# Optimization experiments

Measured on AMD Instinct MI355X. Metric: run time of the kernel, lower is better.

## Reference

```python
import jax, jax.numpy as jnp
import numpy as np

N = 100000   # nodes
E = 1600000  # edges
D = 64       # hidden_channels (heads=1, concat)
NEG_SLOPE = 0.2


def setup_inputs() -> dict:
    key = jax.random.key(0)
    ks = jax.random.split(key, 16)
    s = (1.0 / np.sqrt(D)).astype(np.float32) if hasattr(np.sqrt(D), 'astype') else 1.0 / np.sqrt(D)
    s = 1.0 / float(np.sqrt(D))
    inp = {
        "x": jax.random.normal(ks[0], (N, D), jnp.float32),
        "edge_index": jax.random.randint(ks[1], (2, E), 0, N, dtype=jnp.int32).astype(jnp.int64),
        "edge_attr": jax.random.normal(ks[2], (E, 1), jnp.float32),
        # layer 1 params (PyG GATConv, heads=1): lin, lin_edge, att_src, att_dst, att_edge, bias
        "W1":  jax.random.normal(ks[3], (D, D), jnp.float32) * s,
        "We1": jax.random.normal(ks[4], (1, D), jnp.float32) * s,
        "as1": jax.random.normal(ks[5], (D,), jnp.float32) * s,
        "ad1": jax.random.normal(ks[6], (D,), jnp.float32) * s,
        "ae1": jax.random.normal(ks[7], (D,), jnp.float32) * s,
        "b1":  jnp.zeros((D,), jnp.float32),
        # layer 2 params
        "W2":  jax.random.normal(ks[8], (D, D), jnp.float32) * s,
        "We2": jax.random.normal(ks[9], (1, D), jnp.float32) * s,
        "as2": jax.random.normal(ks[10], (D,), jnp.float32) * s,
        "ad2": jax.random.normal(ks[11], (D,), jnp.float32) * s,
        "ae2": jax.random.normal(ks[12], (D,), jnp.float32) * s,
        "b2":  jnp.zeros((D,), jnp.float32),
    }
    return inp


def _gat_layer(x, src, dst, edge_attr, W, We, a_src, a_dst, a_edge, bias):
    """PyG GATConv, heads=1, add_self_loops=False, edge_dim=1."""
    n = x.shape[0]
    h = x @ W                      # [N, D]  transformed node features
    he = edge_attr @ We            # [E, D]  transformed edge features
    # per-node attention logits, gathered per edge
    alpha = ((h * a_src).sum(-1)[src]
             + (h * a_dst).sum(-1)[dst]
             + (he * a_edge).sum(-1))               # [E]
    alpha = jax.nn.leaky_relu(alpha, NEG_SLOPE)
    # segment softmax over incoming edges of each dst node
    m = jax.ops.segment_max(alpha, dst, num_segments=n)   # [N]
    m = jnp.where(jnp.isfinite(m), m, 0.0)
    e = jnp.exp(alpha - m[dst])                            # [E]
    denom = jax.ops.segment_sum(e, dst, num_segments=n) + 1e-16
    w = e / denom[dst]                                     # [E]
    # weighted scatter-add aggregation of source features
    out = jax.ops.segment_sum(h[src] * w[:, None], dst, num_segments=n)
    return out + bias


def reference(x, edge_index, edge_attr,
              W1, We1, as1, ad1, ae1, b1,
              W2, We2, as2, ad2, ae2, b2):
    src = edge_index[0]
    dst = edge_index[1]
    h = _gat_layer(x, src, dst, edge_attr, W1, We1, as1, ad1, ae1, b1)
    h = jax.nn.relu(h)
    out = _gat_layer(h, src, dst, edge_attr, W2, We2, as2, ad2, ae2, b2)
    return out
```

## Files before the change

### kernel.cpp

```cpp
#include <hip/hip_runtime.h>
#include <hip/hip_fp16.h>
#include <stdint.h>

#define D 64
constexpr float NEG_SLOPE = 0.2f;
#define NPB_SHIFT 9
#define NPB 512
#define PCHUNK 4096

__global__ void k_ce(const float* __restrict__ We1, const float* __restrict__ ae1,
                     const float* __restrict__ We2, const float* __restrict__ ae2,
                     float* __restrict__ ce){
  int lane = threadIdx.x;
  float p1 = We1[lane] * ae1[lane];
  float p2 = We2[lane] * ae2[lane];
  #pragma unroll
  for (int off = 32; off; off >>= 1){ p1 += __shfl_xor(p1, off); p2 += __shfl_xor(p2, off); }
  if (lane == 0){ ce[0] = p1; ce[1] = p2; }
}

__global__ __launch_bounds__(256) void k_gemm_dots(
    const float* __restrict__ X, const float* __restrict__ W,
    const float* __restrict__ a_s, const float* __restrict__ a_d,
    __half* __restrict__ H, float* __restrict__ asrc, float* __restrict__ adst, int n)
{
  __shared__ float sX[4 * 512];
  int lane = threadIdx.x & 63;
  int wv   = threadIdx.x >> 6;
  float* tile = sX + wv * 512;
  int wid  = blockIdx.x * 4 + wv;
  int nw   = gridDim.x * 4;
  float Wc[64];
  #pragma unroll
  for (int k = 0; k < 64; ++k) Wc[k] = W[k * D + lane];
  float asv = a_s[lane], adv = a_d[lane];
  int ngrp = (n + 7) >> 3;
  for (int g = wid; g < ngrp; g += nw){
    int r0 = g << 3;
    if (r0 + 8 <= n){
      const float4* Xg = (const float4*)(X + (size_t)r0 * D);
      float4 t0 = Xg[lane * 2], t1 = Xg[lane * 2 + 1];
      ((float4*)tile)[lane * 2]     = t0;
      ((float4*)tile)[lane * 2 + 1] = t1;
      __builtin_amdgcn_wave_barrier();
      float acc[8];
      #pragma unroll
      for (int j = 0; j < 8; ++j) acc[j] = 0.f;
      #pragma unroll
      for (int j = 0; j < 8; ++j){
        #pragma unroll
        for (int kb = 0; kb < 16; ++kb){
          float4 xv = ((const float4*)(tile + j * 64))[kb];
          acc[j] = fmaf(xv.x, Wc[kb * 4 + 0], acc[j]);
          acc[j] = fmaf(xv.y, Wc[kb * 4 + 1], acc[j]);
          acc[j] = fmaf(xv.z, Wc[kb * 4 + 2], acc[j]);
          acc[j] = fmaf(xv.w, Wc[kb * 4 + 3], acc[j]);
        }
      }
      #pragma unroll
      for (int j = 0; j < 8; ++j) H[(size_t)(r0 + j) * D + lane] = __float2half(acc[j]);
      #pragma unroll
      for (int j = 0; j < 8; ++j){
        float ps = acc[j] * asv, pd = acc[j] * adv;
        #pragma unroll
        for (int off = 32; off; off >>= 1){ ps += __shfl_xor(ps, off); pd += __shfl_xor(pd, off); }
        if (lane == 0){ asrc[r0 + j] = ps; adst[r0 + j] = pd; }
      }
    } else {
      for (int j = 0; r0 + j < n; ++j){
        float acc = 0.f;
        #pragma unroll
        for (int kb = 0; kb < 16; ++kb){
          float4 xv = *(const float4*)(X + (size_t)(r0 + j) * D + kb * 4);
          acc = fmaf(xv.x, Wc[kb * 4 + 0], acc);
          acc = fmaf(xv.y, Wc[kb * 4 + 1], acc);
          acc = fmaf(xv.z, Wc[kb * 4 + 2], acc);
          acc = fmaf(xv.w, Wc[kb * 4 + 3], acc);
        }
        H[(size_t)(r0 + j) * D + lane] = __float2half(acc);
        float ps = acc * asv, pd = acc * adv;
        #pragma unroll
        for (int off = 32; off; off >>= 1){ ps += __shfl_xor(ps, off); pd += __shfl_xor(pd, off); }
        if (lane == 0){ asrc[r0 + j] = ps; adst[r0 + j] = pd; }
      }
    }
  }
}


__global__ __launch_bounds__(256) void k_bhist(const int* __restrict__ dst,
    int* __restrict__ C, int nchunk, int e, int nbkt){
  __shared__ int hist[256];
  int tid = threadIdx.x, c = blockIdx.x;
  if (tid < nbkt) hist[tid] = 0;
  __syncthreads();
  int c0 = c * PCHUNK;
  #pragma unroll
  for (int k = 0; k < PCHUNK / 256; ++k){
    int i = c0 + tid + (k << 8);
    if (i < e) atomicAdd(&hist[dst[i] >> NPB_SHIFT], 1);
  }
  __syncthreads();
  if (tid < nbkt) C[tid * nchunk + c] = hist[tid];
}

__global__ __launch_bounds__(512) void k_cscan(int* __restrict__ C,
    int* __restrict__ btot, int nchunk){
  __shared__ int s[512];
  int b = blockIdx.x, tid = threadIdx.x;
  int v = (tid < nchunk) ? C[b * nchunk + tid] : 0;
  s[tid] = v; __syncthreads();
  #pragma unroll
  for (int off = 1; off < 512; off <<= 1){
    int t = (tid >= off) ? s[tid - off] : 0;
    __syncthreads();
    s[tid] += t;
    __syncthreads();
  }
  if (tid < nchunk) C[b * nchunk + tid] = s[tid] - v;
  if (tid == 511) btot[b] = s[511];
}

__global__ __launch_bounds__(256) void k_bscan(const int* __restrict__ btot,
    int* __restrict__ gbase, int nbkt){
  __shared__ int s[256];
  int tid = threadIdx.x;
  int v = (tid < nbkt) ? btot[tid] : 0;
  s[tid] = v; __syncthreads();
  #pragma unroll
  for (int off = 1; off < 256; off <<= 1){
    int t = (tid >= off) ? s[tid - off] : 0;
    __syncthreads();
    s[tid] += t;
    __syncthreads();
  }
  if (tid < nbkt) gbase[tid] = s[tid] - v;
  if (tid == 255) gbase[nbkt] = s[255];
}

__global__ __launch_bounds__(256) void k_part(const int* __restrict__ src,
    const int* __restrict__ dst, const float* __restrict__ ea,
    const int* __restrict__ gbase, const int* __restrict__ C, int nchunk,
    int2* __restrict__ staging, int e, int nbkt){
  __shared__ int base[256], cnt[256];
  int tid = threadIdx.x, c = blockIdx.x;
  if (tid < nbkt){ base[tid] = gbase[tid] + C[tid * nchunk + c]; cnt[tid] = 0; }
  __syncthreads();
  int c0 = c * PCHUNK;
  int w0[PCHUNK / 256], w1[PCHUNK / 256], bk[PCHUNK / 256];
  #pragma unroll
  for (int k = 0; k < PCHUNK / 256; ++k){
    int i = c0 + tid + (k << 8);
    bk[k] = -1;
    if (i < e){
      int d = dst[i];
      bk[k] = d >> NPB_SHIFT;
      w0[k] = src[i] | ((d & (NPB - 1)) << 17);
      w1[k] = __float_as_int(ea[i]);
    }
  }
  #pragma unroll
  for (int k = 0; k < PCHUNK / 256; ++k){
    if (bk[k] >= 0){
      int pos = base[bk[k]] + atomicAdd(&cnt[bk[k]], 1);
      staging[pos] = make_int2(w0[k], w1[k]);
    }
  }
}

__global__ __launch_bounds__(512) void k_bucket(const int* __restrict__ gbase,
    const int2* __restrict__ staging, int2* __restrict__ edges,
    int* __restrict__ rowptr, int n, int nbkt){
  __shared__ int degL[NPB], sc[NPB];
  int b = blockIdx.x, tid = threadIdx.x;
  int node0 = b << NPB_SHIFT;
  int nn = min(NPB, n - node0);
  int base = gbase[b], endj = gbase[b + 1];
  degL[tid] = 0;
  __syncthreads();
  for (int j = base + tid; j < endj; j += NPB)
    atomicAdd(&degL[staging[j].x >> 17], 1);
  __syncthreads();
  int dv = degL[tid];
  sc[tid] = dv;
  __syncthreads();
  #pragma unroll
  for (int off = 1; off < NPB; off <<= 1){
    int t = (tid >= off) ? sc[tid - off] : 0;
    __syncthreads();
    sc[tid] += t;
    __syncthreads();
  }
  int ex = sc[tid] - dv;
  if (tid < nn) rowptr[node0 + tid] = base + ex;
  if (b == nbkt - 1 && tid == 0) rowptr[n] = base + sc[NPB - 1];
  __syncthreads();
  degL[tid] = ex;
  __syncthreads();
  for (int j = base + tid; j < endj; j += NPB){
    int2 w = staging[j];
    int dloc = w.x >> 17;
    int pos = base + atomicAdd(&degL[dloc], 1);
    edges[pos] = make_int2(w.x & 0x1FFFF, w.y);
  }
}

__global__ __launch_bounds__(256) void k_node_fused(
    const int* __restrict__ rowptr, const int2* __restrict__ edges,
    const float* __restrict__ asrc, const float* __restrict__ adst,
    const float* __restrict__ ce, int ce_idx,
    const __half* __restrict__ H, const float* __restrict__ bias,
    float* __restrict__ out, int n, int relu)
{
  int lane = threadIdx.x & 63;
  int wv   = threadIdx.x >> 6;
  int vbase = (blockIdx.x * 4 + wv) * 2;
  if (vbase >= n) return;
  int h  = lane >> 5;
  int li = lane & 31;
  int v  = vbase + h;
  bool vok = v < n;
  int start = 0, end = 0;
  if (vok){ start = rowptr[v]; end = rowptr[v + 1]; }
  int deg = end - start;
  int degmax = max(deg, __shfl_xor(deg, 32));
  float cev = ce[ce_idx];

  if (degmax <= 32){
    int my_s = 0; float my_e = 0.f;
    if (li < deg){
      int2 pr = edges[start + li];
      my_s = pr.x;
      float a = asrc[pr.x] + adst[v] + __int_as_float(pr.y) * cev;
      a = a > 0.f ? a : NEG_SLOPE * a;
      my_e = __expf(a);
    }
    int sub = li >> 4;
    int fq  = li & 15;
    const uint2* H2 = (const uint2*)H;
    int eb = h * 32 + sub;
    int sP[8]; float wP[8]; uint2 uP[8];
    #pragma unroll
    for (int p = 0; p < 8; ++p) sP[p] = __shfl(my_s, eb + 2 * p);
    #pragma unroll
    for (int p = 0; p < 8; ++p) uP[p] = H2[(size_t)sP[p] * 16 + fq];
    float ss = my_e;
    #pragma unroll
    for (int off = 16; off; off >>= 1) ss += __shfl_xor(ss, off);
    float inv = 1.f / (ss + 1e-16f);
    #pragma unroll
    for (int p = 0; p < 8; ++p) wP[p] = __shfl(my_e, eb + 2 * p);
    float a0 = 0.f, a1 = 0.f, a2 = 0.f, a3 = 0.f;
    #pragma unroll
    for (int p = 0; p < 8; ++p){
      __half2 q0 = *(const __half2*)&uP[p].x;
      __half2 q1 = *(const __half2*)&uP[p].y;
      float2 f0 = __half22float2(q0);
      float2 f1 = __half22float2(q1);
      a0 = fmaf(f0.x, wP[p], a0);
      a1 = fmaf(f0.y, wP[p], a1);
      a2 = fmaf(f1.x, wP[p], a2);
      a3 = fmaf(f1.y, wP[p], a3);
    }
    if (degmax > 16){
      #pragma unroll
      for (int p = 0; p < 8; ++p) sP[p] = __shfl(my_s, eb + 16 + 2 * p);
      #pragma unroll
      for (int p = 0; p < 8; ++p) uP[p] = H2[(size_t)sP[p] * 16 + fq];
      #pragma unroll
      for (int p = 0; p < 8; ++p) wP[p] = __shfl(my_e, eb + 16 + 2 * p);
      #pragma unroll
      for (int p = 0; p < 8; ++p){
        __half2 q0 = *(const __half2*)&uP[p].x;
        __half2 q1 = *(const __half2*)&uP[p].y;
        float2 f0 = __half22float2(q0);
        float2 f1 = __half22float2(q1);
        a0 = fmaf(f0.x, wP[p], a0);
        a1 = fmaf(f0.y, wP[p], a1);
        a2 = fmaf(f1.x, wP[p], a2);
        a3 = fmaf(f1.y, wP[p], a3);
      }
    }
    a0 += __shfl_xor(a0, 16);
    a1 += __shfl_xor(a1, 16);
    a2 += __shfl_xor(a2, 16);
    a3 += __shfl_xor(a3, 16);
    if (vok && li < 16){
      float4 bv = ((const float4*)bias)[li];
      float4 r;
      r.x = a0 * inv + bv.x;
      r.y = a1 * inv + bv.y;
      r.z = a2 * inv + bv.z;
      r.w = a3 * inv + bv.w;
      if (relu){
        r.x = fmaxf(r.x, 0.f); r.y = fmaxf(r.y, 0.f);
        r.z = fmaxf(r.z, 0.f); r.w = fmaxf(r.w, 0.f);
      }
      ((float4*)(out + (size_t)v * D))[li] = r;
    }
  } else {
    for (int t = 0; t < 2; ++t){
      int vv = vbase + t;
      if (vv >= n) break;
      int st = rowptr[vv], en = rowptr[vv + 1];
      int dg = en - st;
      if (dg == 0){
        float bv = bias[lane];
        float r = relu ? fmaxf(bv, 0.f) : bv;
        out[(size_t)vv * D + lane] = r;
        continue;
      }
      float adv = adst[vv];
      if (dg <= 64){
        int my_s = 0; float my_e = 0.f;
        if (lane < dg){
          int2 pr = edges[st + lane];
          my_s = pr.x;
          float a = asrc[pr.x] + adv + __int_as_float(pr.y) * cev;
          a = a > 0.f ? a : NEG_SLOPE * a;
          my_e = __expf(a);
        }
        int hf = lane >> 5;
        int fp = lane & 31;
        const __half2* Hp = (const __half2*)H;
        float ss = my_e;
        #pragma unroll
        for (int off = 32; off; off >>= 1) ss += __shfl_xor(ss, off);
        float inv = 1.f / (ss + 1e-16f);
        float accx = 0.f, accy = 0.f;
        for (int k = 0; k < dg; k += 16){
          #pragma unroll
          for (int p = 0; p < 8; ++p){
            int ix = k + 2 * p + hf; ix = ix > 63 ? 63 : ix;
            int s0 = __shfl(my_s, ix);
            float w0 = __shfl(my_e, ix);
            float2 hv = __half22float2(Hp[(size_t)s0 * 32 + fp]);
            accx = fmaf(hv.x, w0, accx);
            accy = fmaf(hv.y, w0, accy);
          }
        }
        accx += __shfl_xor(accx, 32);
        accy += __shfl_xor(accy, 32);
        if (lane < 32){
          float2 bv2 = ((const float2*)bias)[fp];
          float2 r;
          r.x = accx * inv + bv2.x;
          r.y = accy * inv + bv2.y;
          if (relu){ r.x = fmaxf(r.x, 0.f); r.y = fmaxf(r.y, 0.f); }
          ((float2*)(out + (size_t)vv * D))[fp] = r;
        }
      } else {
        float bv = bias[lane];
        float c0 = 0.f, c1 = 0.f, c2 = 0.f, c3 = 0.f;
        float ss = 0.f;
        for (int j0 = st; j0 < en; j0 += 64){
          int j = j0 + lane;
          int my_s = 0; float my_e = 0.f;
          if (j < en){
            int2 pr = edges[j];
            float a = asrc[pr.x] + adv + __int_as_float(pr.y) * cev;
            a = a > 0.f ? a : NEG_SLOPE * a;
            my_e = __expf(a);
            my_s = pr.x;
          }
          ss += my_e;
          int cnt = min(64, en - j0);
          int k = 0;
          for (; k + 4 <= cnt; k += 4){
            int s0 = __shfl(my_s, k+0), s1 = __shfl(my_s, k+1);
            int s2 = __shfl(my_s, k+2), s3 = __shfl(my_s, k+3);
            float w0 = __shfl(my_e, k+0), w1 = __shfl(my_e, k+1);
            float w2 = __shfl(my_e, k+2), w3 = __shfl(my_e, k+3);
            float h0 = __half2float(H[(size_t)s0 * D + lane]);
            float h1 = __half2float(H[(size_t)s1 * D + lane]);
            float h2 = __half2float(H[(size_t)s2 * D + lane]);
            float h3 = __half2float(H[(size_t)s3 * D + lane]);
            c0 = fmaf(h0, w0, c0); c1 = fmaf(h1, w1, c1);
            c2 = fmaf(h2, w2, c2); c3 = fmaf(h3, w3, c3);
          }
          for (; k < cnt; ++k){
            int s0 = __shfl(my_s, k);
            float w0 = __shfl(my_e, k);
            c0 = fmaf(__half2float(H[(size_t)s0 * D + lane]), w0, c0);
          }
        }
        #pragma unroll
        for (int off = 32; off; off >>= 1) ss += __shfl_xor(ss, off);
        float inv = 1.f / (ss + 1e-16f);
        float acc = (c0 + c1) + (c2 + c3);
        float r = acc * inv + bv;
        if (relu) r = fmaxf(r, 0.f);
        out[(size_t)vv * D + lane] = r;
      }
    }
  }
}

extern "C" void kernel_launch(void* const* d_in, const int* in_sizes, int n_in,
                              void* d_out, int out_size, void* d_ws, size_t ws_size,
                              hipStream_t stream)
{
  const float* x    = (const float*)d_in[0];
  const int*   ei   = (const int*)d_in[1];
  const float* ea   = (const float*)d_in[2];
  const float* W1   = (const float*)d_in[3];
  const float* We1  = (const float*)d_in[4];
  const float* as1  = (const float*)d_in[5];
  const float* ad1  = (const float*)d_in[6];
  const float* ae1  = (const float*)d_in[7];
  const float* b1   = (const float*)d_in[8];
  const float* W2   = (const float*)d_in[9];
  const float* We2  = (const float*)d_in[10];
  const float* as2  = (const float*)d_in[11];
  const float* ad2  = (const float*)d_in[12];
  const float* ae2  = (const float*)d_in[13];
  const float* b2   = (const float*)d_in[14];
  float* out = (float*)d_out;

  int n = in_sizes[0] / D;
  int e = in_sizes[1] / 2;
  const int* srcp = ei;
  const int* dstp = ei + e;

  int nbkt   = (n + NPB - 1) / NPB;
  int nchunk = (e + PCHUNK - 1) / PCHUNK;

  char* p = (char*)d_ws;
  __half* buf_h  = (__half*)p; p += (size_t)n * D * 2;
  float* buf_x2  = (float*)p;  p += (size_t)n * D * 4;
  float* asrc    = (float*)p;  p += (size_t)n * 4;
  float* adst    = (float*)p;  p += (size_t)n * 4;
  int*   rowptr  = (int*)p;    p += (size_t)(n + 16) * 4;
  int*   gbase   = (int*)p;    p += (size_t)(nbkt + 4) * 4;
  int*   btot    = (int*)p;    p += (size_t)(nbkt + 4) * 4;
  int*   C       = (int*)p;    p += (size_t)nbkt * nchunk * 4;
  float* ce      = (float*)p;  p += 64;
  int2*  edges   = (int2*)p;   p += (size_t)e * 8;
  int2*  staging = (int2*)buf_x2;

  int pairs = (n + 1) / 2;
  int gR = (pairs + 3) / 4;
  int gG = ((n + 7) / 8 + 3) / 4;

  k_ce<<<1, 64, 0, stream>>>(We1, ae1, We2, ae2, ce);
  k_bhist<<<nchunk, 256, 0, stream>>>(dstp, C, nchunk, e, nbkt);
  k_cscan<<<nbkt, 512, 0, stream>>>(C, btot, nchunk);
  k_bscan<<<1, 256, 0, stream>>>(btot, gbase, nbkt);
  k_part<<<nchunk, 256, 0, stream>>>(srcp, dstp, ea, gbase, C, nchunk, staging, e, nbkt);
  k_bucket<<<nbkt, NPB, 0, stream>>>(gbase, staging, edges, rowptr, n, nbkt);

  k_gemm_dots<<<gG, 256, 0, stream>>>(x, W1, as1, ad1, buf_h, asrc, adst, n);
  k_node_fused<<<gR, 256, 0, stream>>>(rowptr, edges, asrc, adst, ce, 0, buf_h, b1, buf_x2, n, 1);

  k_gemm_dots<<<gG, 256, 0, stream>>>(buf_x2, W2, as2, ad2, buf_h, asrc, adst, n);
  k_node_fused<<<gR, 256, 0, stream>>>(rowptr, edges, asrc, adst, ce, 1, buf_h, b2, out, n, 0);
}
```

Measured before the change: 281.5 us.

## Fuse layer-2 projection into aggregation epilogue and merge front preprocessing kernels

The first-layer aggregation kernel now keeps each node's output row in shared memory and immediately multiplies it by W2. It writes the half-precision H2 and the layer-2 attention dots directly, which drops the fp32 intermediate buffer and the second GEMM kernel. The layer-1 GEMM, the destination histogram and the edge-constant computation are merged into one launch split by block ranges. The bucket-total scan folds into the chunk-scan kernel through a last-block-done atomic counter. This cuts kernel launches and global traffic, at the cost of per-wave W2 reads from global memory inside the aggregation kernel and a larger grid-wide atomic handoff.

After: 352.0 us. 25.1% more time.

```diff
diff --git a/kernel.cpp b/kernel.cpp
--- a/kernel.cpp
+++ b/kernel.cpp
@@ -8,105 +8,111 @@
 #define NPB 512
 #define PCHUNK 4096
 
-__global__ void k_ce(const float* __restrict__ We1, const float* __restrict__ ae1,
-                     const float* __restrict__ We2, const float* __restrict__ ae2,
-                     float* __restrict__ ce){
-  int lane = threadIdx.x;
-  float p1 = We1[lane] * ae1[lane];
-  float p2 = We2[lane] * ae2[lane];
-  #pragma unroll
-  for (int off = 32; off; off >>= 1){ p1 += __shfl_xor(p1, off); p2 += __shfl_xor(p2, off); }
-  if (lane == 0){ ce[0] = p1; ce[1] = p2; }
-}
-
-__global__ __launch_bounds__(256) void k_gemm_dots(
+__global__ __launch_bounds__(256) void k_front(
     const float* __restrict__ X, const float* __restrict__ W,
     const float* __restrict__ a_s, const float* __restrict__ a_d,
-    __half* __restrict__ H, float* __restrict__ asrc, float* __restrict__ adst, int n)
+    __half* __restrict__ H, float* __restrict__ asrc, float* __restrict__ adst,
+    int n, int gemmBlocks,
+    const int* __restrict__ dst, int* __restrict__ C, int nchunk, int e, int nbkt,
+    const float* __restrict__ We1, const float* __restrict__ ae1,
+    const float* __restrict__ We2, const float* __restrict__ ae2,
+    float* __restrict__ ce, int* __restrict__ done)
 {
   __shared__ float sX[4 * 512];
-  int lane = threadIdx.x & 63;
-  int wv   = threadIdx.x >> 6;
-  float* tile = sX + wv * 512;
-  int wid  = blockIdx.x * 4 + wv;
-  int nw   = gridDim.x * 4;
-  float Wc[64];
-  #pragma unroll
-  for (int k = 0; k < 64; ++k) Wc[k] = W[k * D + lane];
-  float asv = a_s[lane], adv = a_d[lane];
-  int ngrp = (n + 7) >> 3;
-  for (int g = wid; g < ngrp; g += nw){
-    int r0 = g << 3;
-    if (r0 + 8 <= n){
-      const float4* Xg = (const float4*)(X + (size_t)r0 * D);
-      float4 t0 = Xg[lane * 2], t1 = Xg[lane * 2 + 1];
-      ((float4*)tile)[lane * 2]     = t0;
-      ((float4*)tile)[lane * 2 + 1] = t1;
-      __builtin_amdgcn_wave_barrier();
-      float acc[8];
+  int b = blockIdx.x;
+  if (b < gemmBlocks){
+    int lane = threadIdx.x & 63;
+    int wv   = threadIdx.x >> 6;
+    float* tile = sX + wv * 512;
+    int wid  = b * 4 + wv;
+    int nw   = gemmBlocks * 4;
+    float Wc[64];
+    #pragma unroll
+    for (int k = 0; k < 64; ++k) Wc[k] = W[k * D + lane];
+    float asv = a_s[lane], adv = a_d[lane];
+    int ngrp = (n + 7) >> 3;
+    for (int g = wid; g < ngrp; g += nw){
+      int r0 = g << 3;
+      if (r0 + 8 <= n){
+        const float4* Xg = (const float4*)(X + (size_t)r0 * D);
+        float4 t0 = Xg[lane * 2], t1 = Xg[lane * 2 + 1];
+        ((float4*)tile)[lane * 2]     = t0;
+        ((float4*)tile)[lane * 2 + 1] = t1;
+        __builtin_amdgcn_wave_barrier();
+        float acc[8];
+        #pragma unroll
+        for (int j = 0; j < 8; ++j) acc[j] = 0.f;
+        #pragma unroll
+        for (int j = 0; j < 8; ++j){
+          #pragma unroll
+          for (int kb = 0; kb < 16; ++kb){
+            float4 xv = ((const float4*)(tile + j * 64))[kb];
+            acc[j] = fmaf(xv.x, Wc[kb * 4 + 0], acc[j]);
+            acc[j] = fmaf(xv.y, Wc[kb * 4 + 1], acc[j]);
+            acc[j] = fmaf(xv.z, Wc[kb * 4 + 2], acc[j]);
+            acc[j] = fmaf(xv.w, Wc[kb * 4 + 3], acc[j]);
+          }
+        }
+        #pragma unroll
+        for (int j = 0; j < 8; ++j) H[(size_t)(r0 + j) * D + lane] = __float2half(acc[j]);
+        #pragma unroll
+        for (int j = 0; j < 8; ++j){
+          float ps = acc[j] * asv, pd = acc[j] * adv;
+          #pragma unroll
+          for (int off = 32; off; off >>= 1){ ps += __shfl_xor(ps, off); pd += __shfl_xor(pd, off); }
+          if (lane == 0){ asrc[r0 + j] = ps; adst[r0 + j] = pd; }
+        }
+      } else {
+        for (int j = 0; r0 + j < n; ++j){
+          float acc = 0.f;
+          #pragma unroll
+          for (int kb = 0; kb < 16; ++kb){
+            float4 xv = *(const float4*)(X + (size_t)(r0 + j) * D + kb * 4);
+            acc = fmaf(xv.x, Wc[kb * 4 + 0], acc);
+            acc = fmaf(xv.y, Wc[kb * 4 + 1], acc);
+            acc = fmaf(xv.z, Wc[kb * 4 + 2], acc);
+            acc = fmaf(xv.w, Wc[kb * 4 + 3], acc);
+          }
+          H[(size_t)(r0 + j) * D + lane] = __float2half(acc);
+          float ps = acc * asv, pd = acc * adv;
+          #pragma unroll
+          for (int off = 32; off; off >>= 1){ ps += __shfl_xor(ps, off); pd += __shfl_xor(pd, off); }
+          if (lane == 0){ asrc[r0 + j] = ps; adst[r0 + j] = pd; }
+        }
+      }
+    }
+  } else if (b < gemmBlocks + nchunk){
+    int* hist = (int*)sX;
+    int tid = threadIdx.x, c = b - gemmBlocks;
+    if (tid < nbkt) hist[tid] = 0;
+    __syncthreads();
+    int c0 = c * PCHUNK;
+    #pragma unroll
+    for (int k = 0; k < PCHUNK / 256; ++k){
+      int i = c0 + tid + (k << 8);
+      if (i < e) atomicAdd(&hist[dst[i] >> NPB_SHIFT], 1);
+    }
+    __syncthreads();
+    if (tid < nbkt) C[tid * nchunk + c] = hist[tid];
+  } else {
+    int tid = threadIdx.x;
+    if (tid < 64){
+      float p1 = We1[tid] * ae1[tid];
+      float p2 = We2[tid] * ae2[tid];
       #pragma unroll
-      for (int j = 0; j < 8; ++j) acc[j] = 0.f;
-      #pragma unroll
-      for (int j = 0; j < 8; ++j){
-        #pragma unroll
-        for (int kb = 0; kb < 16; ++kb){
-          float4 xv = ((const float4*)(tile + j * 64))[kb];
-          acc[j] = fmaf(xv.x, Wc[kb * 4 + 0], acc[j]);
-          acc[j] = fmaf(xv.y, Wc[kb * 4 + 1], acc[j]);
-          acc[j] = fmaf(xv.z, Wc[kb * 4 + 2], acc[j]);
-          acc[j] = fmaf(xv.w, Wc[kb * 4 + 3], acc[j]);
-        }
-      }
-      #pragma unroll
-      for (int j = 0; j < 8; ++j) H[(size_t)(r0 + j) * D + lane] = __float2half(acc[j]);
-      #pragma unroll
-      for (int j = 0; j < 8; ++j){
-        float ps = acc[j] * asv, pd = acc[j] * adv;
-        #pragma unroll
-        for (int off = 32; off; off >>= 1){ ps += __shfl_xor(ps, off); pd += __shfl_xor(pd, off); }
-        if (lane == 0){ asrc[r0 + j] = ps; adst[r0 + j] = pd; }
-      }
-    } else {
-      for (int j = 0; r0 + j < n; ++j){
-        float acc = 0.f;
-        #pragma unroll
-        for (int kb = 0; kb < 16; ++kb){
-          float4 xv = *(const float4*)(X + (size_t)(r0 + j) * D + kb * 4);
-          acc = fmaf(xv.x, Wc[kb * 4 + 0], acc);
-          acc = fmaf(xv.y, Wc[kb * 4 + 1], acc);
-          acc = fmaf(xv.z, Wc[kb * 4 + 2], acc);
-          acc = fmaf(xv.w, Wc[kb * 4 + 3], acc);
-        }
-        H[(size_t)(r0 + j) * D + lane] = __float2half(acc);
-        float ps = acc * asv, pd = acc * adv;
-        #pragma unroll
-        for (int off = 32; off; off >>= 1){ ps += __shfl_xor(ps, off); pd += __shfl_xor(pd, off); }
-        if (lane == 0){ asrc[r0 + j] = ps; adst[r0 + j] = pd; }
-      }
+      for (int off = 32; off; off >>= 1){ p1 += __shfl_xor(p1, off); p2 += __shfl_xor(p2, off); }
+      if (tid == 0){ ce[0] = p1; ce[1] = p2; }
+    } else if (tid == 64){
+      *done = 0;
     }
   }
 }
 
-
-__global__ __launch_bounds__(256) void k_bhist(const int* __restrict__ dst,
-    int* __restrict__ C, int nchunk, int e, int nbkt){
-  __shared__ int hist[256];
-  int tid = threadIdx.x, c = blockIdx.x;
-  if (tid < nbkt) hist[tid] = 0;
-  __syncthreads();
-  int c0 = c * PCHUNK;
-  #pragma unroll
-  for (int k = 0; k < PCHUNK / 256; ++k){
-    int i = c0 + tid + (k << 8);
-    if (i < e) atomicAdd(&hist[dst[i] >> NPB_SHIFT], 1);
-  }
-  __syncthreads();
-  if (tid < nbkt) C[tid * nchunk + c] = hist[tid];
-}
-
 __global__ __launch_bounds__(512) void k_cscan(int* __restrict__ C,
-    int* __restrict__ btot, int nchunk){
+    int* __restrict__ btot, int* __restrict__ gbase, int* __restrict__ done,
+    int nchunk, int nbkt){
   __shared__ int s[512];
+  __shared__ int amLast;
   int b = blockIdx.x, tid = threadIdx.x;
   int v = (tid < nchunk) ? C[b * nchunk + tid] : 0;
   s[tid] = v; __syncthreads();
@@ -119,23 +125,22 @@
   }
   if (tid < nchunk) C[b * nchunk + tid] = s[tid] - v;
   if (tid == 511) btot[b] = s[511];
-}
-
-__global__ __launch_bounds__(256) void k_bscan(const int* __restrict__ btot,
-    int* __restrict__ gbase, int nbkt){
-  __shared__ int s[256];
-  int tid = threadIdx.x;
-  int v = (tid < nbkt) ? btot[tid] : 0;
-  s[tid] = v; __syncthreads();
+  __threadfence();
+  if (tid == 0) amLast = (atomicAdd(done, 1) == (int)gridDim.x - 1);
+  __syncthreads();
+  if (!amLast) return;
+  __threadfence();
+  int v2 = (tid < nbkt) ? btot[tid] : 0;
+  s[tid] = v2; __syncthreads();
   #pragma unroll
-  for (int off = 1; off < 256; off <<= 1){
+  for (int off = 1; off < 512; off <<= 1){
     int t = (tid >= off) ? s[tid - off] : 0;
     __syncthreads();
     s[tid] += t;
     __syncthreads();
   }
-  if (tid < nbkt) gbase[tid] = s[tid] - v;
-  if (tid == 255) gbase[nbkt] = s[255];
+  if (tid < nbkt) gbase[tid] = s[tid] - v2;
+  if (tid == 511) gbase[nbkt] = s[511];
 }
 
 __global__ __launch_bounds__(256) void k_part(const int* __restrict__ src,
@@ -210,8 +215,12 @@
     const float* __restrict__ asrc, const float* __restrict__ adst,
     const float* __restrict__ ce, int ce_idx,
     const __half* __restrict__ H, const float* __restrict__ bias,
-    float* __restrict__ out, int n, int relu)
+    float* __restrict__ out, int n, int relu,
+    const float* __restrict__ Wn, const float* __restrict__ a_sn,
+    const float* __restrict__ a_dn, __half* __restrict__ Hn,
+    float* __restrict__ asrcn, float* __restrict__ adstn)
 {
+  __shared__ float rowL[4][2][64];
   int lane = threadIdx.x & 63;
   int wv   = threadIdx.x >> 6;
   int vbase = (blockIdx.x * 4 + wv) * 2;
@@ -285,7 +294,7 @@
     a1 += __shfl_xor(a1, 16);
     a2 += __shfl_xor(a2, 16);
     a3 += __shfl_xor(a3, 16);
-    if (vok && li < 16){
+    if (li < 16){
       float4 bv = ((const float4*)bias)[li];
       float4 r;
       r.x = a0 * inv + bv.x;
@@ -296,7 +305,11 @@
         r.x = fmaxf(r.x, 0.f); r.y = fmaxf(r.y, 0.f);
         r.z = fmaxf(r.z, 0.f); r.w = fmaxf(r.w, 0.f);
       }
-      ((float4*)(out + (size_t)v * D))[li] = r;
+      if (Wn){
+        *(float4*)&rowL[wv][h][li * 4] = r;
+      } else if (vok){
+        ((float4*)(out + (size_t)v * D))[li] = r;
+      }
     }
   } else {
     for (int t = 0; t < 2; ++t){
@@ -307,7 +320,8 @@
       if (dg == 0){
         float bv = bias[lane];
         float r = relu ? fmaxf(bv, 0.f) : bv;
-        out[(size_t)vv * D + lane] = r;
+        if (Wn) rowL[wv][t][lane] = r;
+        else    out[(size_t)vv * D + lane] = r;
         continue;
       }
       float adv = adst[vv];
@@ -347,7 +361,11 @@
           r.x = accx * inv + bv2.x;
           r.y = accy * inv + bv2.y;
           if (relu){ r.x = fmaxf(r.x, 0.f); r.y = fmaxf(r.y, 0.f); }
-          ((float2*)(out + (size_t)vv * D))[fp] = r;
+          if (Wn){
+            *(float2*)&rowL[wv][t][fp * 2] = r;
+          } else {
+            ((float2*)(out + (size_t)vv * D))[fp] = r;
+          }
         }
       } else {
         float bv = bias[lane];
@@ -390,8 +408,38 @@
         float acc = (c0 + c1) + (c2 + c3);
         float r = acc * inv + bv;
         if (relu) r = fmaxf(r, 0.f);
-        out[(size_t)vv * D + lane] = r;
+        if (Wn) rowL[wv][t][lane] = r;
+        else    out[(size_t)vv * D + lane] = r;
       }
+    }
+  }
+
+  if (Wn){
+    __builtin_amdgcn_wave_barrier();
+    const float2* W2f2 = (const float2*)Wn;
+    const float4* rowq = (const float4*)rowL[wv][h];
+    float cx = 0.f, cy = 0.f;
+    #pragma unroll
+    for (int db = 0; db < 16; ++db){
+      float4 rq = rowq[db];
+      float2 wa = W2f2[(db * 4 + 0) * 32 + li];
+      float2 wb = W2f2[(db * 4 + 1) * 32 + li];
+      float2 wc = W2f2[(db * 4 + 2) * 32 + li];
+      float2 wd = W2f2[(db * 4 + 3) * 32 + li];
+      cx = fmaf(rq.x, wa.x, cx); cy = fmaf(rq.x, wa.y, cy);
+      cx = fmaf(rq.y, wb.x, cx); cy = fmaf(rq.y, wb.y, cy);
+      cx = fmaf(rq.z, wc.x, cx); cy = fmaf(rq.z, wc.y, cy);
+      cx = fmaf(rq.w, wd.x, cx); cy = fmaf(rq.w, wd.y, cy);
+    }
+    float2 av = ((const float2*)a_sn)[li];
+    float2 dv = ((const float2*)a_dn)[li];
+    float ps = cx * av.x + cy * av.y;
+    float pd = cx * dv.x + cy * dv.y;
+    #pragma unroll
+    for (int off = 16; off; off >>= 1){ ps += __shfl_xor(ps, off); pd += __shfl_xor(pd, off); }
+    if (vok){
+      ((__half2*)Hn)[(size_t)v * 32 + li] = __floats2half2_rn(cx, cy);
+      if (li == 0){ asrcn[v] = ps; adstn[v] = pd; }
     }
   }
 }
@@ -426,32 +474,34 @@
   int nchunk = (e + PCHUNK - 1) / PCHUNK;
 
   char* p = (char*)d_ws;
-  __half* buf_h  = (__half*)p; p += (size_t)n * D * 2;
-  float* buf_x2  = (float*)p;  p += (size_t)n * D * 4;
-  float* asrc    = (float*)p;  p += (size_t)n * 4;
-  float* adst    = (float*)p;  p += (size_t)n * 4;
+  __half* buf_h1 = (__half*)p; p += (size_t)n * D * 2;
+  __half* buf_h2 = (__half*)p; p += (size_t)n * D * 2;
+  float* asrc1   = (float*)p;  p += (size_t)n * 4;
+  float* adst1   = (float*)p;  p += (size_t)n * 4;
+  float* asrc2   = (float*)p;  p += (size_t)n * 4;
+  float* adst2   = (float*)p;  p += (size_t)n * 4;
   int*   rowptr  = (int*)p;    p += (size_t)(n + 16) * 4;
   int*   gbase   = (int*)p;    p += (size_t)(nbkt + 4) * 4;
   int*   btot    = (int*)p;    p += (size_t)(nbkt + 4) * 4;
   int*   C       = (int*)p;    p += (size_t)nbkt * nchunk * 4;
   float* ce      = (float*)p;  p += 64;
+  int*   done    = (int*)p;    p += 64;
   int2*  edges   = (int2*)p;   p += (size_t)e * 8;
-  int2*  staging = (int2*)buf_x2;
+  int2*  staging = (int2*)buf_h2;
 
   int pairs = (n + 1) / 2;
   int gR = (pairs + 3) / 4;
   int gG = ((n + 7) / 8 + 3) / 4;
 
-  k_ce<<<1, 64, 0, stream>>>(We1, ae1, We2, ae2, ce);
-  k_bhist<<<nchunk, 256, 0, stream>>>(dstp, C, nchunk, e, nbkt);
-  k_cscan<<<nbkt, 512, 0, stream>>>(C, btot, nchunk);
-  k_bscan<<<1, 256, 0, stream>>>(btot, gbase, nbkt);
+  k_front<<<gG + nchunk + 1, 256, 0, stream>>>(
+      x, W1, as1, ad1, buf_h1, asrc1, adst1, n, gG,
+      dstp, C, nchunk, e, nbkt, We1, ae1, We2, ae2, ce, done);
+  k_cscan<<<nbkt, 512, 0, stream>>>(C, btot, gbase, done, nchunk, nbkt);
   k_part<<<nchunk, 256, 0, stream>>>(srcp, dstp, ea, gbase, C, nchunk, staging, e, nbkt);
   k_bucket<<<nbkt, NPB, 0, stream>>>(gbase, staging, edges, rowptr, n, nbkt);
 
-  k_gemm_dots<<<gG, 256, 0, stream>>>(x, W1, as1, ad1, buf_h, asrc, adst, n);
-  k_node_fused<<<gR, 256, 0, stream>>>(rowptr, edges, asrc, adst, ce, 0, buf_h, b1, buf_x2, n, 1);
-
-  k_gemm_dots<<<gG, 256, 0, stream>>>(buf_x2, W2, as2, ad2, buf_h, asrc, adst, n);
-  k_node_fused<<<gR, 256, 0, stream>>>(rowptr, edges, asrc, adst, ce, 1, buf_h, b2, out, n, 0);
+  k_node_fused<<<gR, 256, 0, stream>>>(rowptr, edges, asrc1, adst1, ce, 0,
+      buf_h1, b1, nullptr, n, 1, W2, as2, ad2, buf_h2, asrc2, adst2);
+  k_node_fused<<<gR, 256, 0, stream>>>(rowptr, edges, asrc2, adst2, ce, 1,
+      buf_h2, b2, out, n, 0, nullptr, nullptr, nullptr, nullptr, nullptr, nullptr);
 }
```

## Replace two-level bucket partition CSR build with global atomic degree count and scatter

Applied to the files above, without the earlier changes.

Replaces the bucketed CSR construction (per-chunk histograms, chunk scan, partition into staging, per-bucket local sort) with a simpler pipeline. The new pipeline zeroes a degree array, counts degrees with global atomics, runs a two-pass decoupled scan whose last block finishes the block sums, and scatters edges using global atomic cursors. It is meant to cut the staging round-trip and several kernel launches. In exchange it relies on many contended global atomics with random scatter writes, and the order of edges within a row becomes nondeterministic, which can change floating-point summation order.

Result: slower. 455.4 us (+61.8%).

```diff
diff --git a/kernel.cpp b/kernel.cpp
--- a/kernel.cpp
+++ b/kernel.cpp
@@ -4,19 +4,100 @@
 
 #define D 64
 constexpr float NEG_SLOPE = 0.2f;
-#define NPB_SHIFT 9
-#define NPB 512
-#define PCHUNK 4096
-
-__global__ void k_ce(const float* __restrict__ We1, const float* __restrict__ ae1,
-                     const float* __restrict__ We2, const float* __restrict__ ae2,
-                     float* __restrict__ ce){
-  int lane = threadIdx.x;
-  float p1 = We1[lane] * ae1[lane];
-  float p2 = We2[lane] * ae2[lane];
+
+__global__ __launch_bounds__(256) void k_init(
+    int* __restrict__ deg, int n, int* __restrict__ done,
+    const float* __restrict__ We1, const float* __restrict__ ae1,
+    const float* __restrict__ We2, const float* __restrict__ ae2,
+    float* __restrict__ ce)
+{
+  int i = blockIdx.x * 256 + threadIdx.x;
+  int stride = gridDim.x * 256;
+  for (; i < n; i += stride) deg[i] = 0;
+  if (blockIdx.x == 0){
+    int tid = threadIdx.x;
+    if (tid < 64){
+      float p1 = We1[tid] * ae1[tid];
+      float p2 = We2[tid] * ae2[tid];
+      #pragma unroll
+      for (int off = 32; off; off >>= 1){ p1 += __shfl_xor(p1, off); p2 += __shfl_xor(p2, off); }
+      if (tid == 0){ ce[0] = p1; ce[1] = p2; }
+    } else if (tid == 64){
+      *done = 0;
+    }
+  }
+}
+
+__global__ __launch_bounds__(256) void k_deg(const int* __restrict__ dst,
+    int* __restrict__ deg, int e)
+{
+  int i = blockIdx.x * 256 + threadIdx.x;
+  int stride = gridDim.x * 256;
+  for (; i < e; i += stride) atomicAdd(&deg[dst[i]], 1);
+}
+
+__global__ __launch_bounds__(512) void k_scan1(const int* __restrict__ deg,
+    int* __restrict__ rowptr, int* __restrict__ bsum, int* __restrict__ done,
+    int n, int nblk)
+{
+  __shared__ int s[512];
+  __shared__ int amLast;
+  int b = blockIdx.x, tid = threadIdx.x;
+  int v = b * 512 + tid;
+  int val = (v < n) ? deg[v] : 0;
+  s[tid] = val; __syncthreads();
   #pragma unroll
-  for (int off = 32; off; off >>= 1){ p1 += __shfl_xor(p1, off); p2 += __shfl_xor(p2, off); }
-  if (lane == 0){ ce[0] = p1; ce[1] = p2; }
+  for (int off = 1; off < 512; off <<= 1){
+    int t = (tid >= off) ? s[tid - off] : 0;
+    __syncthreads();
+    s[tid] += t;
+    __syncthreads();
+  }
+  if (v < n) rowptr[v] = s[tid] - val;
+  if (tid == 511) bsum[b] = s[511];
+  __threadfence();
+  if (tid == 0) amLast = (atomicAdd(done, 1) == nblk - 1);
+  __syncthreads();
+  if (!amLast) return;
+  __threadfence();
+  int v2 = (tid < nblk) ? bsum[tid] : 0;
+  s[tid] = v2; __syncthreads();
+  #pragma unroll
+  for (int off = 1; off < 512; off <<= 1){
+    int t = (tid >= off) ? s[tid - off] : 0;
+    __syncthreads();
+    s[tid] += t;
+    __syncthreads();
+  }
+  if (tid < nblk) bsum[tid] = s[tid] - v2;
+}
+
+__global__ __launch_bounds__(512) void k_scan2(int* __restrict__ rowptr,
+    int* __restrict__ cursor, const int* __restrict__ bsum, int n, int e)
+{
+  int b = blockIdx.x, tid = threadIdx.x;
+  int v = b * 512 + tid;
+  if (v < n){
+    int r = rowptr[v] + bsum[b];
+    rowptr[v] = r;
+    cursor[v] = r;
+  }
+  if (b == 0 && tid == 0) rowptr[n] = e;
+}
+
+__global__ __launch_bounds__(256) void k_scatter(const int* __restrict__ src,
+    const int* __restrict__ dst, const float* __restrict__ ea,
+    int* __restrict__ cursor, int2* __restrict__ edges, int e)
+{
+  int i = blockIdx.x * 256 + threadIdx.x;
+  int stride = gridDim.x * 256;
+  for (; i < e; i += stride){
+    int d = dst[i];
+    int sv = src[i];
+    float av = ea[i];
+    int pos = atomicAdd(&cursor[d], 1);
+    edges[pos] = make_int2(sv, __float_as_int(av));
+  }
 }
 
 __global__ __launch_bounds__(256) void k_gemm_dots(
@@ -84,124 +165,6 @@
         if (lane == 0){ asrc[r0 + j] = ps; adst[r0 + j] = pd; }
       }
     }
-  }
-}
-
-
-__global__ __launch_bounds__(256) void k_bhist(const int* __restrict__ dst,
-    int* __restrict__ C, int nchunk, int e, int nbkt){
-  __shared__ int hist[256];
-  int tid = threadIdx.x, c = blockIdx.x;
-  if (tid < nbkt) hist[tid] = 0;
-  __syncthreads();
-  int c0 = c * PCHUNK;
-  #pragma unroll
-  for (int k = 0; k < PCHUNK / 256; ++k){
-    int i = c0 + tid + (k << 8);
-    if (i < e) atomicAdd(&hist[dst[i] >> NPB_SHIFT], 1);
-  }
-  __syncthreads();
-  if (tid < nbkt) C[tid * nchunk + c] = hist[tid];
-}
-
-__global__ __launch_bounds__(512) void k_cscan(int* __restrict__ C,
-    int* __restrict__ btot, int nchunk){
-  __shared__ int s[512];
-  int b = blockIdx.x, tid = threadIdx.x;
-  int v = (tid < nchunk) ? C[b * nchunk + tid] : 0;
-  s[tid] = v; __syncthreads();
-  #pragma unroll
-  for (int off = 1; off < 512; off <<= 1){
-    int t = (tid >= off) ? s[tid - off] : 0;
-    __syncthreads();
-    s[tid] += t;
-    __syncthreads();
-  }
-  if (tid < nchunk) C[b * nchunk + tid] = s[tid] - v;
-  if (tid == 511) btot[b] = s[511];
-}
-
-__global__ __launch_bounds__(256) void k_bscan(const int* __restrict__ btot,
-    int* __restrict__ gbase, int nbkt){
-  __shared__ int s[256];
-  int tid = threadIdx.x;
-  int v = (tid < nbkt) ? btot[tid] : 0;
-  s[tid] = v; __syncthreads();
-  #pragma unroll
-  for (int off = 1; off < 256; off <<= 1){
-    int t = (tid >= off) ? s[tid - off] : 0;
-    __syncthreads();
-    s[tid] += t;
-    __syncthreads();
-  }
-  if (tid < nbkt) gbase[tid] = s[tid] - v;
-  if (tid == 255) gbase[nbkt] = s[255];
-}
-
-__global__ __launch_bounds__(256) void k_part(const int* __restrict__ src,
-    const int* __restrict__ dst, const float* __restrict__ ea,
-    const int* __restrict__ gbase, const int* __restrict__ C, int nchunk,
-    int2* __restrict__ staging, int e, int nbkt){
-  __shared__ int base[256], cnt[256];
-  int tid = threadIdx.x, c = blockIdx.x;
-  if (tid < nbkt){ base[tid] = gbase[tid] + C[tid * nchunk + c]; cnt[tid] = 0; }
-  __syncthreads();
-  int c0 = c * PCHUNK;
-  int w0[PCHUNK / 256], w1[PCHUNK / 256], bk[PCHUNK / 256];
-  #pragma unroll
-  for (int k = 0; k < PCHUNK / 256; ++k){
-    int i = c0 + tid + (k << 8);
-    bk[k] = -1;
-    if (i < e){
-      int d = dst[i];
-      bk[k] = d >> NPB_SHIFT;
-      w0[k] = src[i] | ((d & (NPB - 1)) << 17);
-      w1[k] = __float_as_int(ea[i]);
-    }
-  }
-  #pragma unroll
-  for (int k = 0; k < PCHUNK / 256; ++k){
-    if (bk[k] >= 0){
-      int pos = base[bk[k]] + atomicAdd(&cnt[bk[k]], 1);
-      staging[pos] = make_int2(w0[k], w1[k]);
-    }
-  }
-}
-
-__global__ __launch_bounds__(512) void k_bucket(const int* __restrict__ gbase,
-    const int2* __restrict__ staging, int2* __restrict__ edges,
-    int* __restrict__ rowptr, int n, int nbkt){
-  __shared__ int degL[NPB], sc[NPB];
-  int b = blockIdx.x, tid = threadIdx.x;
-  int node0 = b << NPB_SHIFT;
-  int nn = min(NPB, n - node0);
-  int base = gbase[b], endj = gbase[b + 1];
-  degL[tid] = 0;
-  __syncthreads();
-  for (int j = base + tid; j < endj; j += NPB)
-    atomicAdd(&degL[staging[j].x >> 17], 1);
-  __syncthreads();
-  int dv = degL[tid];
-  sc[tid] = dv;
-  __syncthreads();
-  #pragma unroll
-  for (int off = 1; off < NPB; off <<= 1){
-    int t = (tid >= off) ? sc[tid - off] : 0;
-    __syncthreads();
-    sc[tid] += t;
-    __syncthreads();
-  }
-  int ex = sc[tid] - dv;
-  if (tid < nn) rowptr[node0 + tid] = base + ex;
-  if (b == nbkt - 1 && tid == 0) rowptr[n] = base + sc[NPB - 1];
-  __syncthreads();
-  degL[tid] = ex;
-  __syncthreads();
-  for (int j = base + tid; j < endj; j += NPB){
-    int2 w = staging[j];
-    int dloc = w.x >> 17;
-    int pos = base + atomicAdd(&degL[dloc], 1);
-    edges[pos] = make_int2(w.x & 0x1FFFF, w.y);
   }
 }
 
@@ -422,8 +385,7 @@
   const int* srcp = ei;
   const int* dstp = ei + e;
 
-  int nbkt   = (n + NPB - 1) / NPB;
-  int nchunk = (e + PCHUNK - 1) / PCHUNK;
+  int nblk = (n + 511) / 512;
 
   char* p = (char*)d_ws;
   __half* buf_h  = (__half*)p; p += (size_t)n * D * 2;
@@ -431,27 +393,27 @@
   float* asrc    = (float*)p;  p += (size_t)n * 4;
   float* adst    = (float*)p;  p += (size_t)n * 4;
   int*   rowptr  = (int*)p;    p += (size_t)(n + 16) * 4;
-  int*   gbase   = (int*)p;    p += (size_t)(nbkt + 4) * 4;
-  int*   btot    = (int*)p;    p += (size_t)(nbkt + 4) * 4;
-  int*   C       = (int*)p;    p += (size_t)nbkt * nchunk * 4;
+  int*   deg     = (int*)p;    p += (size_t)(n + 16) * 4;
+  int*   cursor  = (int*)p;    p += (size_t)(n + 16) * 4;
+  int*   bsum    = (int*)p;    p += 512 * 4;
   float* ce      = (float*)p;  p += 64;
+  int*   done    = (int*)p;    p += 64;
   int2*  edges   = (int2*)p;   p += (size_t)e * 8;
-  int2*  staging = (int2*)buf_x2;
 
   int pairs = (n + 1) / 2;
   int gR = (pairs + 3) / 4;
   int gG = ((n + 7) / 8 + 3) / 4;
 
-  k_ce<<<1, 64, 0, stream>>>(We1, ae1, We2, ae2, ce);
-  k_bhist<<<nchunk, 256, 0, stream>>>(dstp, C, nchunk, e, nbkt);
-  k_cscan<<<nbkt, 512, 0, stream>>>(C, btot, nchunk);
-  k_bscan<<<1, 256, 0, stream>>>(btot, gbase, nbkt);
-  k_part<<<nchunk, 256, 0, stream>>>(srcp, dstp, ea, gbase, C, nchunk, staging, e, nbkt);
-  k_bucket<<<nbkt, NPB, 0, stream>>>(gbase, staging, edges, rowptr, n, nbkt);
+  k_init<<<256, 256, 0, stream>>>(deg, n, done, We1, ae1, We2, ae2, ce);
+  k_deg<<<1024, 256, 0, stream>>>(dstp, deg, e);
+  k_scan1<<<nblk, 512, 0, stream>>>(deg, rowptr, bsum, done, n, nblk);
+  k_scan2<<<nblk, 512, 0, stream>>>(rowptr, cursor, bsum, n, e);
+  k_scatter<<<1024, 256, 0, stream>>>(srcp, dstp, ea, cursor, edges, e);
 
   k_gemm_dots<<<gG, 256, 0, stream>>>(x, W1, as1, ad1, buf_h, asrc, adst, n);
-  k_node_fused<<<gR, 256, 0, stream>>>(rowptr, edges, asrc, adst, ce, 0, buf_h, b1, buf_x2, n, 1);
-
+  k_node_fused<<<gR, 256, 0, stream>>>(rowptr, edges, asrc, adst, ce, 0,
+      buf_h, b1, buf_x2, n, 1);
   k_gemm_dots<<<gG, 256, 0, stream>>>(buf_x2, W2, as2, ad2, buf_h, asrc, adst, n);
-  k_node_fused<<<gR, 256, 0, stream>>>(rowptr, edges, asrc, adst, ce, 1, buf_h, b2, out, n, 0);
-}
+  k_node_fused<<<gR, 256, 0, stream>>>(rowptr, edges, asrc, adst, ce, 1,
+      buf_h, b2, out, n, 0);
+}
```

## Map four nodes per wavefront in aggregation and widen partition blocks to 512

Applied to the files above, without the earlier changes.

The fused GAT aggregation kernel now gives each node 16 lanes, so one wavefront handles four destination nodes instead of two. Each lane owns a fixed 4-feature slice and walks edges serially in groups of eight. This removes the cross-half reduction and halves the number of waves. In exchange, the long-tail branch for degrees above 16 or 32 fires more often, because it is now decided by the maximum degree over four nodes. Separately, the histogram and partition kernels use 512-thread blocks with fewer items per thread.

Measured after the change: 284.1 us. About the same (+0.9%).

```diff
diff --git a/kernel.cpp b/kernel.cpp
--- a/kernel.cpp
+++ b/kernel.cpp
@@ -88,7 +88,7 @@
 }
 
 
-__global__ __launch_bounds__(256) void k_bhist(const int* __restrict__ dst,
+__global__ __launch_bounds__(512) void k_bhist(const int* __restrict__ dst,
     int* __restrict__ C, int nchunk, int e, int nbkt){
   __shared__ int hist[256];
   int tid = threadIdx.x, c = blockIdx.x;
@@ -96,8 +96,8 @@
   __syncthreads();
   int c0 = c * PCHUNK;
   #pragma unroll
-  for (int k = 0; k < PCHUNK / 256; ++k){
-    int i = c0 + tid + (k << 8);
+  for (int k = 0; k < PCHUNK / 512; ++k){
+    int i = c0 + tid + (k << 9);
     if (i < e) atomicAdd(&hist[dst[i] >> NPB_SHIFT], 1);
   }
   __syncthreads();
@@ -138,7 +138,7 @@
   if (tid == 255) gbase[nbkt] = s[255];
 }
 
-__global__ __launch_bounds__(256) void k_part(const int* __restrict__ src,
+__global__ __launch_bounds__(512) void k_part(const int* __restrict__ src,
     const int* __restrict__ dst, const float* __restrict__ ea,
     const int* __restrict__ gbase, const int* __restrict__ C, int nchunk,
     int2* __restrict__ staging, int e, int nbkt){
@@ -147,10 +147,10 @@
   if (tid < nbkt){ base[tid] = gbase[tid] + C[tid * nchunk + c]; cnt[tid] = 0; }
   __syncthreads();
   int c0 = c * PCHUNK;
-  int w0[PCHUNK / 256], w1[PCHUNK / 256], bk[PCHUNK / 256];
-  #pragma unroll
-  for (int k = 0; k < PCHUNK / 256; ++k){
-    int i = c0 + tid + (k << 8);
+  int w0[PCHUNK / 512], w1[PCHUNK / 512], bk[PCHUNK / 512];
+  #pragma unroll
+  for (int k = 0; k < PCHUNK / 512; ++k){
+    int i = c0 + tid + (k << 9);
     bk[k] = -1;
     if (i < e){
       int d = dst[i];
@@ -160,7 +160,7 @@
     }
   }
   #pragma unroll
-  for (int k = 0; k < PCHUNK / 256; ++k){
+  for (int k = 0; k < PCHUNK / 512; ++k){
     if (bk[k] >= 0){
       int pos = base[bk[k]] + atomicAdd(&cnt[bk[k]], 1);
       staging[pos] = make_int2(w0[k], w1[k]);
@@ -214,78 +214,115 @@
 {
   int lane = threadIdx.x & 63;
   int wv   = threadIdx.x >> 6;
-  int vbase = (blockIdx.x * 4 + wv) * 2;
+  int vbase = (blockIdx.x * 4 + wv) * 4;
   if (vbase >= n) return;
-  int h  = lane >> 5;
-  int li = lane & 31;
-  int v  = vbase + h;
+  int q  = lane >> 4;
+  int li = lane & 15;
+  int v  = vbase + q;
   bool vok = v < n;
   int start = 0, end = 0;
   if (vok){ start = rowptr[v]; end = rowptr[v + 1]; }
   int deg = end - start;
-  int degmax = max(deg, __shfl_xor(deg, 32));
+  int dm = deg;
+  dm = max(dm, __shfl_xor(dm, 16));
+  dm = max(dm, __shfl_xor(dm, 32));
   float cev = ce[ce_idx];
 
-  if (degmax <= 32){
-    int my_s = 0; float my_e = 0.f;
+  if (dm <= 32){
+    int s0 = 0, s1 = 0; float e0 = 0.f, e1 = 0.f;
     if (li < deg){
       int2 pr = edges[start + li];
-      my_s = pr.x;
+      s0 = pr.x;
       float a = asrc[pr.x] + adst[v] + __int_as_float(pr.y) * cev;
       a = a > 0.f ? a : NEG_SLOPE * a;
-      my_e = __expf(a);
-    }
-    int sub = li >> 4;
-    int fq  = li & 15;
+      e0 = __expf(a);
+    }
+    if (li + 16 < deg){
+      int2 pr = edges[start + 16 + li];
+      s1 = pr.x;
+      float a = asrc[pr.x] + adst[v] + __int_as_float(pr.y) * cev;
+      a = a > 0.f ? a : NEG_SLOPE * a;
+      e1 = __expf(a);
+    }
     const uint2* H2 = (const uint2*)H;
-    int eb = h * 32 + sub;
-    int sP[8]; float wP[8]; uint2 uP[8];
-    #pragma unroll
-    for (int p = 0; p < 8; ++p) sP[p] = __shfl(my_s, eb + 2 * p);
-    #pragma unroll
-    for (int p = 0; p < 8; ++p) uP[p] = H2[(size_t)sP[p] * 16 + fq];
-    float ss = my_e;
-    #pragma unroll
-    for (int off = 16; off; off >>= 1) ss += __shfl_xor(ss, off);
+    int qb = q << 4;
+    int sP[8]; uint2 uP[8]; float wP[8];
+    float a0 = 0.f, a1 = 0.f, a2 = 0.f, a3 = 0.f;
+    #pragma unroll
+    for (int p = 0; p < 8; ++p) sP[p] = __shfl(s0, qb + p);
+    #pragma unroll
+    for (int p = 0; p < 8; ++p) uP[p] = H2[(size_t)sP[p] * 16 + li];
+    float ss = e0 + e1;
+    #pragma unroll
+    for (int off = 8; off; off >>= 1) ss += __shfl_xor(ss, off);
     float inv = 1.f / (ss + 1e-16f);
     #pragma unroll
-    for (int p = 0; p < 8; ++p) wP[p] = __shfl(my_e, eb + 2 * p);
-    float a0 = 0.f, a1 = 0.f, a2 = 0.f, a3 = 0.f;
+    for (int p = 0; p < 8; ++p) wP[p] = __shfl(e0, qb + p);
     #pragma unroll
     for (int p = 0; p < 8; ++p){
-      __half2 q0 = *(const __half2*)&uP[p].x;
-      __half2 q1 = *(const __half2*)&uP[p].y;
-      float2 f0 = __half22float2(q0);
-      float2 f1 = __half22float2(q1);
+      __half2 h0 = *(const __half2*)&uP[p].x;
+      __half2 h1 = *(const __half2*)&uP[p].y;
+      float2 f0 = __half22float2(h0);
+      float2 f1 = __half22float2(h1);
       a0 = fmaf(f0.x, wP[p], a0);
       a1 = fmaf(f0.y, wP[p], a1);
       a2 = fmaf(f1.x, wP[p], a2);
       a3 = fmaf(f1.y, wP[p], a3);
     }
-    if (degmax > 16){
-      #pragma unroll
-      for (int p = 0; p < 8; ++p) sP[p] = __shfl(my_s, eb + 16 + 2 * p);
-      #pragma unroll
-      for (int p = 0; p < 8; ++p) uP[p] = H2[(size_t)sP[p] * 16 + fq];
-      #pragma unroll
-      for (int p = 0; p < 8; ++p) wP[p] = __shfl(my_e, eb + 16 + 2 * p);
+    #pragma unroll
+    for (int p = 0; p < 8; ++p) sP[p] = __shfl(s0, qb + 8 + p);
+    #pragma unroll
+    for (int p = 0; p < 8; ++p) uP[p] = H2[(size_t)sP[p] * 16 + li];
+    #pragma unroll
+    for (int p = 0; p < 8; ++p) wP[p] = __shfl(e0, qb + 8 + p);
+    #pragma unroll
+    for (int p = 0; p < 8; ++p){
+      __half2 h0 = *(const __half2*)&uP[p].x;
+      __half2 h1 = *(const __half2*)&uP[p].y;
+      float2 f0 = __half22float2(h0);
+      float2 f1 = __half22float2(h1);
+      a0 = fmaf(f0.x, wP[p], a0);
+      a1 = fmaf(f0.y, wP[p], a1);
+      a2 = fmaf(f1.x, wP[p], a2);
+      a3 = fmaf(f1.y, wP[p], a3);
+    }
+    if (dm > 16){
+      #pragma unroll
+      for (int p = 0; p < 8; ++p) sP[p] = __shfl(s1, qb + p);
+      #pragma unroll
+      for (int p = 0; p < 8; ++p) uP[p] = H2[(size_t)sP[p] * 16 + li];
+      #pragma unroll
+      for (int p = 0; p < 8; ++p) wP[p] = __shfl(e1, qb + p);
       #pragma unroll
       for (int p = 0; p < 8; ++p){
-        __half2 q0 = *(const __half2*)&uP[p].x;
-        __half2 q1 = *(const __half2*)&uP[p].y;
-        float2 f0 = __half22float2(q0);
-        float2 f1 = __half22float2(q1);
+        __half2 h0 = *(const __half2*)&uP[p].x;
+        __half2 h1 = *(const __half2*)&uP[p].y;
+        float2 f0 = __half22float2(h0);
+        float2 f1 = __half22float2(h1);
         a0 = fmaf(f0.x, wP[p], a0);
         a1 = fmaf(f0.y, wP[p], a1);
         a2 = fmaf(f1.x, wP[p], a2);
         a3 = fmaf(f1.y, wP[p], a3);
       }
-    }
-    a0 += __shfl_xor(a0, 16);
-    a1 += __shfl_xor(a1, 16);
-    a2 += __shfl_xor(a2, 16);
-    a3 += __shfl_xor(a3, 16);
-    if (vok && li < 16){
+      #pragma unroll
+      for (int p = 0; p < 8; ++p) sP[p] = __shfl(s1, qb + 8 + p);
+      #pragma unroll
+      for (int p = 0; p < 8; ++p) uP[p] = H2[(size_t)sP[p] * 16 + li];
+      #pragma unroll
+      for (int p = 0; p < 8; ++p) wP[p] = __shfl(e1, qb + 8 + p);
+      #pragma unroll
+      for (int p = 0; p < 8; ++p){
+        __half2 h0 = *(const __half2*)&uP[p].x;
+        __half2 h1 = *(const __half2*)&uP[p].y;
+        float2 f0 = __half22float2(h0);
+        float2 f1 = __half22float2(h1);
+        a0 = fmaf(f0.x, wP[p], a0);
+        a1 = fmaf(f0.y, wP[p], a1);
+        a2 = fmaf(f1.x, wP[p], a2);
+        a3 = fmaf(f1.y, wP[p], a3);
+      }
+    }
+    if (vok){
       float4 bv = ((const float4*)bias)[li];
       float4 r;
       r.x = a0 * inv + bv.x;
@@ -299,7 +336,7 @@
       ((float4*)(out + (size_t)v * D))[li] = r;
     }
   } else {
-    for (int t = 0; t < 2; ++t){
+    for (int t = 0; t < 4; ++t){
       int vv = vbase + t;
       if (vv >= n) break;
       int st = rowptr[vv], en = rowptr[vv + 1];
@@ -438,20 +475,21 @@
   int2*  edges   = (int2*)p;   p += (size_t)e * 8;
   int2*  staging = (int2*)buf_x2;
 
-  int pairs = (n + 1) / 2;
-  int gR = (pairs + 3) / 4;
+  int quads = (n + 3) / 4;
+  int gR = (quads + 3) / 4;
   int gG = ((n + 7) / 8 + 3) / 4;
 
   k_ce<<<1, 64, 0, stream>>>(We1, ae1, We2, ae2, ce);
-  k_bhist<<<nchunk, 256, 0, stream>>>(dstp, C, nchunk, e, nbkt);
+  k_bhist<<<nchunk, 512, 0, stream>>>(dstp, C, nchunk, e, nbkt);
   k_cscan<<<nbkt, 512, 0, stream>>>(C, btot, nchunk);
   k_bscan<<<1, 256, 0, stream>>>(btot, gbase, nbkt);
-  k_part<<<nchunk, 256, 0, stream>>>(srcp, dstp, ea, gbase, C, nchunk, staging, e, nbkt);
+  k_part<<<nchunk, 512, 0, stream>>>(srcp, dstp, ea, gbase, C, nchunk, staging, e, nbkt);
   k_bucket<<<nbkt, NPB, 0, stream>>>(gbase, staging, edges, rowptr, n, nbkt);
 
   k_gemm_dots<<<gG, 256, 0, stream>>>(x, W1, as1, ad1, buf_h, asrc, adst, n);
-  k_node_fused<<<gR, 256, 0, stream>>>(rowptr, edges, asrc, adst, ce, 0, buf_h, b1, buf_x2, n, 1);
-
+  k_node_fused<<<gR, 256, 0, stream>>>(rowptr, edges, asrc, adst, ce, 0,
+      buf_h, b1, buf_x2, n, 1);
   k_gemm_dots<<<gG, 256, 0, stream>>>(buf_x2, W2, as2, ad2, buf_h, asrc, adst, n);
-  k_node_fused<<<gR, 256, 0, stream>>>(rowptr, edges, asrc, adst, ce, 1, buf_h, b2, out, n, 0);
-}
+  k_node_fused<<<gR, 256, 0, stream>>>(rowptr, edges, asrc, adst, ce, 1,
+      buf_h, b2, out, n, 0);
+}
```
